# Optimization experiments

Measured on AMD Instinct MI355X. Metric: run time of the kernel, lower is better.

## Reference

```python
import jax, jax.numpy as jnp
import numpy as np
import math

N_HEAD = 16
D_MODEL = 1024
KSIZE = 3
PAD = 1


def _conv1d(x, w, b, pad):
    # x: [B, C_in, S], w: [C_out, C_in, K] (torch Conv1d layout)
    y = jax.lax.conv_general_dilated(
        x, w, window_strides=(1,), padding=[(pad, pad)],
        dimension_numbers=("NCH", "OIH", "NCH"))
    return y + b[None, :, None]


def setup_inputs() -> dict:
    key = jax.random.key(0)
    ks = jax.random.split(key, 10)
    B, S, D = 2, 2048, D_MODEL
    sc = 1.0 / math.sqrt(D)
    return {
        "q": jax.random.normal(ks[0], (B, S, D), jnp.float32),
        "k": jax.random.normal(ks[1], (B, S, D), jnp.float32),
        "v": jax.random.normal(ks[2], (B, S, D), jnp.float32),
        "wq_w": jax.random.normal(ks[3], (D, D, KSIZE), jnp.float32) * sc,
        "wq_b": jnp.zeros((D,), jnp.float32),
        "wk_w": jax.random.normal(ks[4], (D, D, KSIZE), jnp.float32) * sc,
        "wk_b": jnp.zeros((D,), jnp.float32),
        "wv_w": jax.random.normal(ks[5], (D, D, 1), jnp.float32) * sc,
        "wv_b": jnp.zeros((D,), jnp.float32),
        "wc_w": jax.random.normal(ks[6], (D, D), jnp.float32) * sc,
        "wc_b": jnp.zeros((D,), jnp.float32),
    }


def reference(q, k, v, wq_w, wq_b, wk_w, wk_b, wv_w, wv_b, wc_w, wc_b):
    B, S, D = q.shape
    h = N_HEAD
    d = D // h
    # channels-first for conv projections: [B, D, S]
    qc = _conv1d(jnp.swapaxes(q, 1, 2), wq_w, wq_b, PAD)
    kc = _conv1d(jnp.swapaxes(k, 1, 2), wk_w, wk_b, PAD)
    vc = _conv1d(jnp.swapaxes(v, 1, 2), wv_w, wv_b, 0)
    # faithful to torch: view(b, d, h, s) then transpose(1,2).transpose(2,3) -> [b, h, s, d]
    # (head index is the FAST axis of the channel dim, matching the original)
    qh = jnp.transpose(qc.reshape(B, d, h, S), (0, 2, 3, 1))
    kh = jnp.transpose(kc.reshape(B, d, h, S), (0, 2, 3, 1))
    vh = jnp.transpose(vc.reshape(B, d, h, S), (0, 2, 3, 1))
    scores = jnp.einsum("bhqd,bhkd->bhqk", qh, kh) / math.sqrt(d)
    attn = jax.nn.softmax(scores, axis=-1)
    out = jnp.einsum("bhqk,bhkd->bhqd", attn, vh)
    # concat: [b,h,s,d] -> [b,s,h*d]
    out = jnp.transpose(out, (0, 2, 1, 3)).reshape(B, S, D)
    # torch Linear: x @ W^T + b
    return out @ wc_w.T + wc_b
```

## Files before the change

### kernel.cpp

```cpp
#include <hip/hip_runtime.h>
#include <hip/hip_bf16.h>

#define SS 2048
#define DDIM 1024

typedef unsigned short u16;
typedef unsigned int u32;
typedef __attribute__((ext_vector_type(8))) short bf16x8_t;
typedef __attribute__((ext_vector_type(4))) float f32x4_t;

__device__ __forceinline__ u16 f2bf(float f) {
  __hip_bfloat16 h = __float2bfloat16(f);
  return *reinterpret_cast<u16*>(&h);
}

__device__ __forceinline__ void gld16(const void* g, void* lds_base) {
  __builtin_amdgcn_global_load_lds(
      (const __attribute__((address_space(1))) u32*)(uintptr_t)g,
      (__attribute__((address_space(3))) u32*)(u32)(uintptr_t)lds_base,
      16, 0, 0);
}

__global__ void zero_kernel(u32* zb) { zb[threadIdx.x] = 0u; }

__global__ __launch_bounds__(256) void convert3_kernel(
    const float* __restrict__ q, const float* __restrict__ k,
    const float* __restrict__ v, u16* __restrict__ Xq, u16* __restrict__ Xk,
    u16* __restrict__ Xv) {
  const int z = blockIdx.y;
  const float* src = (z == 0) ? q : (z == 1) ? k : v;
  u16* dst = (z == 0) ? Xq : (z == 1) ? Xk : Xv;
  int i = blockIdx.x * 256 + threadIdx.x;
  const float4* s = (const float4*)src + (size_t)i * 2;
  float4 f0 = s[0], f1 = s[1];
  u16 o[8] = {f2bf(f0.x), f2bf(f0.y), f2bf(f0.z), f2bf(f0.w),
              f2bf(f1.x), f2bf(f1.y), f2bf(f1.z), f2bf(f1.w)};
  *(uint4*)(dst + (size_t)i * 8) = *(const uint4*)o;
}

__global__ __launch_bounds__(256) void repack3_kernel(
    const float* __restrict__ wq, const float* __restrict__ wk,
    u16* __restrict__ Wqr, u16* __restrict__ Wkr) {
  const float* w = blockIdx.y ? wk : wq;
  u16* out = blockIdx.y ? Wkr : Wqr;
  int o = blockIdx.x;
  for (int j = threadIdx.x; j < 3072; j += 256) {
    int i = j / 3, t = j - i * 3;
    out[(size_t)o * 3072 + t * 1024 + i] = f2bf(w[(size_t)o * 3072 + j]);
  }
}

__global__ __launch_bounds__(256) void repackc_kernel(
    const float* __restrict__ wv, const float* __restrict__ wc,
    u16* __restrict__ Wvr, u16* __restrict__ Wcr) {
  const float* w = blockIdx.y ? wc : wv;
  u16* out = blockIdx.y ? Wcr : Wvr;
  size_t i = (size_t)blockIdx.x * 1024 + threadIdx.x * 4;
  float4 f = *(const float4*)(w + i);
  u16 o4[4] = {f2bf(f.x), f2bf(f.y), f2bf(f.z), f2bf(f.w)};
  *(ushort4*)(out + i) = *(const ushort4*)o4;
}

__global__ __launch_bounds__(256) void mfma_proj(
    const u16* __restrict__ Xq, const u16* __restrict__ Xk,
    const u16* __restrict__ Xv, const u16* __restrict__ Wq,
    const u16* __restrict__ Wk, const u16* __restrict__ Wv,
    const float* __restrict__ bq, const float* __restrict__ bk,
    const float* __restrict__ bv, u16* __restrict__ Qhb,
    u16* __restrict__ Khb, u16* __restrict__ Vtb,
    const u16* __restrict__ zbuf) {
  __shared__ __attribute__((aligned(16))) u16 As2[2][128][40];
  __shared__ __attribute__((aligned(16))) u16 Bs2[2][128][40];
  const int z = blockIdx.z;
  const u16* __restrict__ Xb = (z == 0) ? Xq : (z == 1) ? Xk : Xv;
  const u16* __restrict__ Wr = (z == 0) ? Wq : (z == 1) ? Wk : Wv;
  const float* __restrict__ bias = (z == 0) ? bq : (z == 1) ? bk : bv;
  u16* __restrict__ Cptr = (z == 0) ? Qhb : (z == 1) ? Khb : Vtb;
  const int nk = (z == 2) ? 32 : 96;
  const bool conv = (z < 2);
  const bool vout = (z == 2);
  const float scale = (z == 0) ? 0.125f : 1.0f;
  const int Kdim = (z == 2) ? 1024 : 3072;

  const int tid = threadIdx.x;
  const int lane = tid & 63;
  const int w = tid >> 6;
  const int ln = tid & 15;
  const int quad = (tid >> 4) & 3;
  const int wrow = w >> 1, wcol = w & 1;
  const int m0 = blockIdx.x * 128, n0 = blockIdx.y * 128;

  auto stage = [&](int ks, int bi) {
    int k0 = ks * 32;
    for (int c = w; c < 10; c += 4) {
      int G = c * 64 + lane;
      int x = G / 5, kb = G - x * 5;
      if (kb < 4) {
        int gm = m0 + x;
        const u16* src;
        if (conv) {
          int b = gm >> 11, s = gm & 2047;
          int t = k0 >> 10;
          int sp = s + t - 1;
          src = (sp >= 0 && sp < SS)
                    ? Xb + ((size_t)(b * SS + sp) * DDIM + (k0 & 1023) + kb * 8)
                    : zbuf;
        } else {
          src = Xb + ((size_t)gm * DDIM + k0 + kb * 8);
        }
        gld16(src, (char*)As2[bi] + c * 1024);
      }
    }
    for (int c = w; c < 10; c += 4) {
      int G = c * 64 + lane;
      int x = G / 5, kb = G - x * 5;
      if (kb < 4)
        gld16(Wr + (size_t)(n0 + x) * Kdim + k0 + kb * 8,
              (char*)Bs2[bi] + c * 1024);
    }
  };

  f32x4_t acc[4][4];
#pragma unroll
  for (int i = 0; i < 4; ++i)
#pragma unroll
    for (int j = 0; j < 4; ++j) acc[i][j] = (f32x4_t){0.f, 0.f, 0.f, 0.f};

  stage(0, 0);
  __syncthreads();

  for (int ks = 0; ks < nk; ++ks) {
    int cur = ks & 1;
    if (ks + 1 < nk) stage(ks + 1, cur ^ 1);

    const u16(*As)[40] = As2[cur];
    const u16(*Bs)[40] = Bs2[cur];
    bf16x8_t a[4], b[4];
#pragma unroll
    for (int mt = 0; mt < 4; ++mt)
      a[mt] = *(const bf16x8_t*)&As[wrow * 64 + mt * 16 + ln][quad * 8];
#pragma unroll
    for (int nt = 0; nt < 4; ++nt)
      b[nt] = *(const bf16x8_t*)&Bs[wcol * 64 + nt * 16 + ln][quad * 8];
#pragma unroll
    for (int mt = 0; mt < 4; ++mt)
#pragma unroll
      for (int nt = 0; nt < 4; ++nt)
        acc[mt][nt] = __builtin_amdgcn_mfma_f32_16x16x32_bf16(
            a[mt], b[nt], acc[mt][nt], 0, 0, 0);

    __syncthreads();
  }

#pragma unroll
  for (int mt = 0; mt < 4; ++mt) {
#pragma unroll
    for (int nt = 0; nt < 4; ++nt) {
      int gn = n0 + wcol * 64 + nt * 16 + ln;
      float bi = bias[gn];
#pragma unroll
      for (int r = 0; r < 4; ++r) {
        int gm = m0 + wrow * 64 + mt * 16 + quad * 4 + r;
        float val = (acc[mt][nt][r] + bi) * scale;
        int b = gm >> 11, s = gm & 2047;
        int hh = gn & 15, dd = gn >> 4;
        if (!vout)
          Cptr[((size_t)(b * 16 + hh) * SS + s) * 64 + dd] = f2bf(val);
        else
          Cptr[((size_t)(b * 16 + hh) * 64 + dd) * SS + s] = f2bf(val);
      }
    }
  }
}

__global__ __launch_bounds__(256) void mfma_gemm_lin(
    const u16* __restrict__ Xb, const u16* __restrict__ Wr,
    const float* __restrict__ bias, float* __restrict__ Cptr) {
  __shared__ __attribute__((aligned(16))) u16 As2[2][32][40];
  __shared__ __attribute__((aligned(16))) u16 Bs2[2][128][40];
  const int tid = threadIdx.x;
  const int lane = tid & 63;
  const int w = tid >> 6;
  const int ln = tid & 15;
  const int quad = (tid >> 4) & 3;
  const int wrow = w >> 1, wcol = w & 1;
  const int m0 = blockIdx.x * 32, n0 = blockIdx.y * 128;

  auto stage = [&](int ks, int bi) {
    int k0 = ks * 32;
    for (int c = w; c < 3; c += 4) {
      int G = c * 64 + lane;
      int x = G / 5, kb = G - x * 5;
      if (kb < 4 && x < 32)
        gld16(Xb + ((size_t)(m0 + x) * DDIM + k0 + kb * 8),
              (char*)As2[bi] + c * 1024);
    }
    for (int c = w; c < 10; c += 4) {
      int G = c * 64 + lane;
      int x = G / 5, kb = G - x * 5;
      if (kb < 4)
        gld16(Wr + (size_t)(n0 + x) * 1024 + k0 + kb * 8,
              (char*)Bs2[bi] + c * 1024);
    }
  };

  f32x4_t acc[4];
#pragma unroll
  for (int j = 0; j < 4; ++j) acc[j] = (f32x4_t){0.f, 0.f, 0.f, 0.f};

  stage(0, 0);
  __syncthreads();

  for (int ks = 0; ks < 32; ++ks) {
    int cur = ks & 1;
    if (ks + 1 < 32) stage(ks + 1, cur ^ 1);

    const u16(*As)[40] = As2[cur];
    const u16(*Bs)[40] = Bs2[cur];
    bf16x8_t a = *(const bf16x8_t*)&As[wrow * 16 + ln][quad * 8];
    bf16x8_t b[4];
#pragma unroll
    for (int nt = 0; nt < 4; ++nt)
      b[nt] = *(const bf16x8_t*)&Bs[wcol * 64 + nt * 16 + ln][quad * 8];
#pragma unroll
    for (int nt = 0; nt < 4; ++nt)
      acc[nt] = __builtin_amdgcn_mfma_f32_16x16x32_bf16(a, b[nt], acc[nt], 0, 0, 0);

    __syncthreads();
  }

#pragma unroll
  for (int nt = 0; nt < 4; ++nt) {
    int gn = n0 + wcol * 64 + nt * 16 + ln;
    float bi = bias[gn];
#pragma unroll
    for (int r = 0; r < 4; ++r) {
      int gm = m0 + wrow * 16 + quad * 4 + r;
      Cptr[(size_t)gm * DDIM + gn] = acc[nt][r] + bi;
    }
  }
}

__global__ __launch_bounds__(256) void mfma_attn(
    const u16* __restrict__ Qhb, const u16* __restrict__ Khb,
    const u16* __restrict__ Vtb, u16* __restrict__ Aob,
    const u16* __restrict__ zbuf) {
  __shared__ __attribute__((aligned(16))) u16 Ks2[2][64][72];
  __shared__ __attribute__((aligned(16))) u16 Vt2[2][64][72];
  __shared__ __attribute__((aligned(16))) u16 Ps[4][16][72];
  const int tid = threadIdx.x;
  const int lane = tid & 63;
  const int w = tid >> 6;
  const int ln = tid & 15;
  const int quad = (tid >> 4) & 3;
  const int bh = blockIdx.y;
  const int b = bh >> 4, hh = bh & 15;
  const int s0 = blockIdx.x * 64;

  auto stage = [&](int kt, int bi) {
    for (int c = w; c < 9; c += 4) {
      int G = c * 64 + lane;
      int x = G / 9, db = G - x * 9;
      if (db < 8) {
        gld16(Khb + ((size_t)bh * SS + kt * 64 + x) * 64 + db * 8,
              (char*)Ks2[bi] + c * 1024);
        gld16(Vtb + ((size_t)bh * 64 + x) * SS + kt * 64 + db * 8,
              (char*)Vt2[bi] + c * 1024);
      }
    }
  };

  const u16* qp = Qhb + ((size_t)bh * SS + s0 + w * 16 + ln) * 64 + quad * 8;
  bf16x8_t qf0 = *(const bf16x8_t*)qp;
  bf16x8_t qf1 = *(const bf16x8_t*)(qp + 32);

  float mrow[4], lsum[4];
  f32x4_t oacc[4];
#pragma unroll
  for (int r = 0; r < 4; ++r) { mrow[r] = -3e38f; lsum[r] = 0.f; }
#pragma unroll
  for (int dt = 0; dt < 4; ++dt) oacc[dt] = (f32x4_t){0.f, 0.f, 0.f, 0.f};

  stage(0, 0);
  __syncthreads();

  for (int kt = 0; kt < 32; ++kt) {
    int cur = kt & 1;
    if (kt + 1 < 32) stage(kt + 1, cur ^ 1);

    const u16(*Ks)[72] = Ks2[cur];
    const u16(*Vt)[72] = Vt2[cur];

    f32x4_t sc[4];
#pragma unroll
    for (int nt = 0; nt < 4; ++nt) sc[nt] = (f32x4_t){0.f, 0.f, 0.f, 0.f};
#pragma unroll
    for (int nt = 0; nt < 4; ++nt) {
      bf16x8_t k0f = *(const bf16x8_t*)&Ks[nt * 16 + ln][quad * 8];
      sc[nt] = __builtin_amdgcn_mfma_f32_16x16x32_bf16(qf0, k0f, sc[nt], 0, 0, 0);
      bf16x8_t k1f = *(const bf16x8_t*)&Ks[nt * 16 + ln][32 + quad * 8];
      sc[nt] = __builtin_amdgcn_mfma_f32_16x16x32_bf16(qf1, k1f, sc[nt], 0, 0, 0);
    }

    float mxv[4];
    bool need = false;
#pragma unroll
    for (int r = 0; r < 4; ++r) {
      float mx = fmaxf(fmaxf(sc[0][r], sc[1][r]), fmaxf(sc[2][r], sc[3][r]));
      mx = fmaxf(mx, __shfl_xor(mx, 1, 64));
      mx = fmaxf(mx, __shfl_xor(mx, 2, 64));
      mx = fmaxf(mx, __shfl_xor(mx, 4, 64));
      mx = fmaxf(mx, __shfl_xor(mx, 8, 64));
      mxv[r] = mx;
      need = need || (mx > mrow[r]);
    }
    if (__any(need)) {
#pragma unroll
      for (int r = 0; r < 4; ++r) {
        float mn = fmaxf(mrow[r], mxv[r]);
        float al = __expf(mrow[r] - mn);
        mrow[r] = mn;
        lsum[r] *= al;
#pragma unroll
        for (int dt = 0; dt < 4; ++dt) oacc[dt][r] *= al;
      }
    }
#pragma unroll
    for (int r = 0; r < 4; ++r) {
      float p0 = __expf(sc[0][r] - mrow[r]), p1 = __expf(sc[1][r] - mrow[r]);
      float p2 = __expf(sc[2][r] - mrow[r]), p3 = __expf(sc[3][r] - mrow[r]);
      lsum[r] += p0 + p1 + p2 + p3;
      Ps[w][quad * 4 + r][ln] = f2bf(p0);
      Ps[w][quad * 4 + r][16 + ln] = f2bf(p1);
      Ps[w][quad * 4 + r][32 + ln] = f2bf(p2);
      Ps[w][quad * 4 + r][48 + ln] = f2bf(p3);
    }

    bf16x8_t pa0 = *(const bf16x8_t*)&Ps[w][ln][quad * 8];
    bf16x8_t pa1 = *(const bf16x8_t*)&Ps[w][ln][32 + quad * 8];
#pragma unroll
    for (int dt = 0; dt < 4; ++dt) {
      bf16x8_t v0f = *(const bf16x8_t*)&Vt[dt * 16 + ln][quad * 8];
      oacc[dt] = __builtin_amdgcn_mfma_f32_16x16x32_bf16(pa0, v0f, oacc[dt], 0, 0, 0);
      bf16x8_t v1f = *(const bf16x8_t*)&Vt[dt * 16 + ln][32 + quad * 8];
      oacc[dt] = __builtin_amdgcn_mfma_f32_16x16x32_bf16(pa1, v1f, oacc[dt], 0, 0, 0);
    }

    __syncthreads();
  }

  float inv[4];
#pragma unroll
  for (int r = 0; r < 4; ++r) {
    float t = lsum[r];
    t += __shfl_xor(t, 1, 64);
    t += __shfl_xor(t, 2, 64);
    t += __shfl_xor(t, 4, 64);
    t += __shfl_xor(t, 8, 64);
    inv[r] = 1.f / t;
  }
#pragma unroll
  for (int dt = 0; dt < 4; ++dt)
#pragma unroll
    for (int r = 0; r < 4; ++r) {
      int gm = b * SS + s0 + w * 16 + quad * 4 + r;
      Aob[(size_t)gm * DDIM + hh * 64 + dt * 16 + ln] = f2bf(oacc[dt][r] * inv[r]);
    }
}

extern "C" void kernel_launch(void* const* d_in, const int* in_sizes, int n_in,
                              void* d_out, int out_size, void* d_ws, size_t ws_size,
                              hipStream_t stream) {
  const float* q    = (const float*)d_in[0];
  const float* k    = (const float*)d_in[1];
  const float* v    = (const float*)d_in[2];
  const float* wq_w = (const float*)d_in[3];
  const float* wq_b = (const float*)d_in[4];
  const float* wk_w = (const float*)d_in[5];
  const float* wk_b = (const float*)d_in[6];
  const float* wv_w = (const float*)d_in[7];
  const float* wv_b = (const float*)d_in[8];
  const float* wc_w = (const float*)d_in[9];
  const float* wc_b = (const float*)d_in[10];

  char* ws = (char*)d_ws;
  size_t off = 0;
  u16* zbuf = (u16*)(ws + off); off += 256;
  const size_t SZ_ACT = (size_t)2 * SS * DDIM * 2;
  u16* Xq  = (u16*)(ws + off); off += SZ_ACT;
  u16* Xk  = (u16*)(ws + off); off += SZ_ACT;
  u16* Xv  = (u16*)(ws + off); off += SZ_ACT;
  u16* Wqr = (u16*)(ws + off); off += (size_t)1024 * 3072 * 2;
  u16* Wkr = (u16*)(ws + off); off += (size_t)1024 * 3072 * 2;
  u16* Wvr = (u16*)(ws + off); off += (size_t)1024 * 1024 * 2;
  u16* Wcr = (u16*)(ws + off); off += (size_t)1024 * 1024 * 2;
  u16* Qhb = (u16*)(ws + off); off += SZ_ACT;
  u16* Khb = (u16*)(ws + off); off += SZ_ACT;
  u16* Vtb = (u16*)(ws + off); off += SZ_ACT;
  u16* Aob = (u16*)(ws + off); off += SZ_ACT;
  if (ws_size < off) return;

  zero_kernel<<<1, 64, 0, stream>>>((u32*)zbuf);
  convert3_kernel<<<dim3(2048, 3), 256, 0, stream>>>(q, k, v, Xq, Xk, Xv);
  repack3_kernel<<<dim3(1024, 2), 256, 0, stream>>>(wq_w, wk_w, Wqr, Wkr);
  repackc_kernel<<<dim3(1024, 2), 256, 0, stream>>>(wv_w, wc_w, Wvr, Wcr);

  mfma_proj<<<dim3(32, 8, 3), 256, 0, stream>>>(
      Xq, Xk, Xv, Wqr, Wkr, Wvr, wq_b, wk_b, wv_b, Qhb, Khb, Vtb, zbuf);

  mfma_attn<<<dim3(32, 32), 256, 0, stream>>>(Qhb, Khb, Vtb, Aob, zbuf);

  mfma_gemm_lin<<<dim3(128, 8), 256, 0, stream>>>(Aob, Wcr, wc_b, (float*)d_out);
}
```

Baseline: 441.3 us.

## Replace syncthreads with partial vmcnt waits so next-tile prefetch overlaps compute

In all three MFMA kernels, each stage's global-to-LDS load loops are merged into one per-wave loop, so every wave knows how many loads it issued. Before each barrier, each wave waits with an explicit s_waitcnt vmcnt(N) that covers only the current tile's loads. This lets the next tile's prefetch stay in flight during the compute, where __syncthreads previously drained all outstanding memory ops. The risk is correctness: the hand-counted vmcnt values must match the exact number of loads each wave issues, and the compiler must not reorder around the inline asm.

```diff
diff --git a/kernel.cpp b/kernel.cpp
--- a/kernel.cpp
+++ b/kernel.cpp
@@ -92,32 +92,34 @@
 
   auto stage = [&](int ks, int bi) {
     int k0 = ks * 32;
-    for (int c = w; c < 10; c += 4) {
-      int G = c * 64 + lane;
-      int x = G / 5, kb = G - x * 5;
-      if (kb < 4) {
-        int gm = m0 + x;
-        const u16* src;
-        if (conv) {
-          int b = gm >> 11, s = gm & 2047;
-          int t = k0 >> 10;
-          int sp = s + t - 1;
-          src = (sp >= 0 && sp < SS)
-                    ? Xb + ((size_t)(b * SS + sp) * DDIM + (k0 & 1023) + kb * 8)
-                    : zbuf;
-        } else {
-          src = Xb + ((size_t)gm * DDIM + k0 + kb * 8);
+    for (int c = w; c < 20; c += 4) {
+      if (c < 10) {
+        int G = c * 64 + lane;
+        int x = G / 5, kb = G - x * 5;
+        if (kb < 4) {
+          int gm = m0 + x;
+          const u16* src;
+          if (conv) {
+            int b = gm >> 11, s = gm & 2047;
+            int t = k0 >> 10;
+            int sp = s + t - 1;
+            src = (sp >= 0 && sp < SS)
+                      ? Xb + ((size_t)(b * SS + sp) * DDIM + (k0 & 1023) + kb * 8)
+                      : zbuf;
+          } else {
+            src = Xb + ((size_t)gm * DDIM + k0 + kb * 8);
+          }
+          gld16(src, (char*)As2[bi] + c * 1024);
         }
-        gld16(src, (char*)As2[bi] + c * 1024);
+      } else {
+        int c2 = c - 10;
+        int G = c2 * 64 + lane;
+        int x = G / 5, kb = G - x * 5;
+        if (kb < 4)
+          gld16(Wr + (size_t)(n0 + x) * Kdim + k0 + kb * 8,
+                (char*)Bs2[bi] + c2 * 1024);
       }
     }
-    for (int c = w; c < 10; c += 4) {
-      int G = c * 64 + lane;
-      int x = G / 5, kb = G - x * 5;
-      if (kb < 4)
-        gld16(Wr + (size_t)(n0 + x) * Kdim + k0 + kb * 8,
-              (char*)Bs2[bi] + c * 1024);
-    }
   };
 
   f32x4_t acc[4][4];
@@ -127,11 +129,18 @@
     for (int j = 0; j < 4; ++j) acc[i][j] = (f32x4_t){0.f, 0.f, 0.f, 0.f};
 
   stage(0, 0);
-  __syncthreads();
 
   for (int ks = 0; ks < nk; ++ks) {
     int cur = ks & 1;
-    if (ks + 1 < nk) stage(ks + 1, cur ^ 1);
+    bool more = (ks + 1 < nk);
+    if (more) {
+      stage(ks + 1, cur ^ 1);
+      asm volatile("s_waitcnt vmcnt(5)" ::: "memory");
+    } else {
+      asm volatile("s_waitcnt vmcnt(0)" ::: "memory");
+    }
+    __builtin_amdgcn_s_barrier();
+    __builtin_amdgcn_sched_barrier(0);
 
     const u16(*As)[40] = As2[cur];
     const u16(*Bs)[40] = Bs2[cur];
@@ -149,7 +158,9 @@
         acc[mt][nt] = __builtin_amdgcn_mfma_f32_16x16x32_bf16(
             a[mt], b[nt], acc[mt][nt], 0, 0, 0);
 
-    __syncthreads();
+    asm volatile("s_waitcnt lgkmcnt(0)" ::: "memory");
+    __builtin_amdgcn_s_barrier();
+    __builtin_amdgcn_sched_barrier(0);
   }
 
 #pragma unroll
@@ -188,19 +199,21 @@
 
   auto stage = [&](int ks, int bi) {
     int k0 = ks * 32;
-    for (int c = w; c < 3; c += 4) {
-      int G = c * 64 + lane;
-      int x = G / 5, kb = G - x * 5;
-      if (kb < 4 && x < 32)
-        gld16(Xb + ((size_t)(m0 + x) * DDIM + k0 + kb * 8),
-              (char*)As2[bi] + c * 1024);
-    }
-    for (int c = w; c < 10; c += 4) {
-      int G = c * 64 + lane;
-      int x = G / 5, kb = G - x * 5;
-      if (kb < 4)
-        gld16(Wr + (size_t)(n0 + x) * 1024 + k0 + kb * 8,
-              (char*)Bs2[bi] + c * 1024);
+    for (int c = w; c < 13; c += 4) {
+      if (c < 3) {
+        int G = c * 64 + lane;
+        int x = G / 5, kb = G - x * 5;
+        if (kb < 4 && x < 32)
+          gld16(Xb + ((size_t)(m0 + x) * DDIM + k0 + kb * 8),
+                (char*)As2[bi] + c * 1024);
+      } else {
+        int c2 = c - 3;
+        int G = c2 * 64 + lane;
+        int x = G / 5, kb = G - x * 5;
+        if (kb < 4)
+          gld16(Wr + (size_t)(n0 + x) * 1024 + k0 + kb * 8,
+                (char*)Bs2[bi] + c2 * 1024);
+      }
     }
   };
 
@@ -209,11 +222,19 @@
   for (int j = 0; j < 4; ++j) acc[j] = (f32x4_t){0.f, 0.f, 0.f, 0.f};
 
   stage(0, 0);
-  __syncthreads();
 
   for (int ks = 0; ks < 32; ++ks) {
     int cur = ks & 1;
-    if (ks + 1 < 32) stage(ks + 1, cur ^ 1);
+    bool more = (ks + 1 < 32);
+    if (more) {
+      stage(ks + 1, cur ^ 1);
+      if (w == 0) asm volatile("s_waitcnt vmcnt(4)" ::: "memory");
+      else        asm volatile("s_waitcnt vmcnt(3)" ::: "memory");
+    } else {
+      asm volatile("s_waitcnt vmcnt(0)" ::: "memory");
+    }
+    __builtin_amdgcn_s_barrier();
+    __builtin_amdgcn_sched_barrier(0);
 
     const u16(*As)[40] = As2[cur];
     const u16(*Bs)[40] = Bs2[cur];
@@ -226,7 +247,9 @@
     for (int nt = 0; nt < 4; ++nt)
       acc[nt] = __builtin_amdgcn_mfma_f32_16x16x32_bf16(a, b[nt], acc[nt], 0, 0, 0);
 
-    __syncthreads();
+    asm volatile("s_waitcnt lgkmcnt(0)" ::: "memory");
+    __builtin_amdgcn_s_barrier();
+    __builtin_amdgcn_sched_barrier(0);
   }
 
 #pragma unroll
@@ -258,14 +281,20 @@
   const int s0 = blockIdx.x * 64;
 
   auto stage = [&](int kt, int bi) {
-    for (int c = w; c < 9; c += 4) {
-      int G = c * 64 + lane;
-      int x = G / 9, db = G - x * 9;
-      if (db < 8) {
-        gld16(Khb + ((size_t)bh * SS + kt * 64 + x) * 64 + db * 8,
-              (char*)Ks2[bi] + c * 1024);
-        gld16(Vtb + ((size_t)bh * 64 + x) * SS + kt * 64 + db * 8,
-              (char*)Vt2[bi] + c * 1024);
+    for (int c = w; c < 18; c += 4) {
+      if (c < 9) {
+        int G = c * 64 + lane;
+        int x = G / 9, db = G - x * 9;
+        if (db < 8)
+          gld16(Khb + ((size_t)bh * SS + kt * 64 + x) * 64 + db * 8,
+                (char*)Ks2[bi] + c * 1024);
+      } else {
+        int c2 = c - 9;
+        int G = c2 * 64 + lane;
+        int x = G / 9, db = G - x * 9;
+        if (db < 8)
+          gld16(Vtb + ((size_t)bh * 64 + x) * SS + kt * 64 + db * 8,
+                (char*)Vt2[bi] + c2 * 1024);
       }
     }
   };
@@ -282,11 +311,19 @@
   for (int dt = 0; dt < 4; ++dt) oacc[dt] = (f32x4_t){0.f, 0.f, 0.f, 0.f};
 
   stage(0, 0);
-  __syncthreads();
 
   for (int kt = 0; kt < 32; ++kt) {
     int cur = kt & 1;
-    if (kt + 1 < 32) stage(kt + 1, cur ^ 1);
+    bool more = (kt + 1 < 32);
+    if (more) {
+      stage(kt + 1, cur ^ 1);
+      if (w < 2) asm volatile("s_waitcnt vmcnt(5)" ::: "memory");
+      else       asm volatile("s_waitcnt vmcnt(4)" ::: "memory");
+    } else {
+      asm volatile("s_waitcnt vmcnt(0)" ::: "memory");
+    }
+    __builtin_amdgcn_s_barrier();
+    __builtin_amdgcn_sched_barrier(0);
 
     const u16(*Ks)[72] = Ks2[cur];
     const u16(*Vt)[72] = Vt2[cur];
@@ -346,7 +383,9 @@
       oacc[dt] = __builtin_amdgcn_mfma_f32_16x16x32_bf16(pa1, v1f, oacc[dt], 0, 0, 0);
     }
 
-    __syncthreads();
+    asm volatile("s_waitcnt lgkmcnt(0)" ::: "memory");
+    __builtin_amdgcn_s_barrier();
+    __builtin_amdgcn_sched_barrier(0);
   }
 
   float inv[4];
```

Result: slower. 504.3 us (+14.3%).
